# Kernel tuning notes

Hardware: AMD Instinct MI355X
Metric: run time of the kernel (lower is better)

The kernel has to match this reference:

```python
import jax, jax.numpy as jnp
import numpy as np
from jax import lax

N_CLASS = 32000
N_HIDDEN = 512
S_ENC = 1024
S_DEC = 256


def setup_inputs() -> dict:
    key = jax.random.key(0)
    ks = jax.random.split(key, 16)
    C, H = N_CLASS, N_HIDDEN
    sC = np.float32(1.0 / np.sqrt(C))
    sH = np.float32(1.0 / np.sqrt(H))
    f32 = jnp.float32
    return {
        "encoder_inputs": jax.random.normal(ks[0], (1, S_ENC, C), f32),
        "hidden_0": jnp.zeros((1, 1, H), f32),
        "decoder_inputs": jax.random.normal(ks[1], (1, S_DEC, C), f32),
        # encoder RNN params (torch nn.RNN layout: W_ih [H,C], W_hh [H,H])
        "enc_Wih": jax.random.normal(ks[2], (H, C), f32) * sC,
        "enc_Whh": jax.random.normal(ks[3], (H, H), f32) * sH,
        "enc_bih": jax.random.normal(ks[4], (H,), f32) * sH,
        "enc_bhh": jax.random.normal(ks[5], (H,), f32) * sH,
        # decoder RNN params
        "dec_Wih": jax.random.normal(ks[6], (H, C), f32) * sC,
        "dec_Whh": jax.random.normal(ks[7], (H, H), f32) * sH,
        "dec_bih": jax.random.normal(ks[8], (H,), f32) * sH,
        "dec_bhh": jax.random.normal(ks[9], (H,), f32) * sH,
        # attention Linear [H,H]
        "attn_W": jax.random.normal(ks[10], (H, H), f32) * sH,
        "attn_b": jax.random.normal(ks[11], (H,), f32) * sH,
        # output Linear [C, 2H]
        "out_W": jax.random.normal(ks[12], (C, 2 * H), f32) * sH,
        "out_b": jax.random.normal(ks[13], (C,), f32) * sH,
    }


def _rnn_scan(x, h0, Wih, Whh, bih, bhh):
    # x: [S, C], h0: [H] -> hs: [S, H], hT: [H]  (tanh vanilla RNN)
    def step(h, xt):
        h = jnp.tanh(xt @ Wih.T + bih + h @ Whh.T + bhh)
        return h, h
    hT, hs = lax.scan(step, h0, x)
    return hs, hT


def reference(encoder_inputs, hidden_0, decoder_inputs,
              enc_Wih, enc_Whh, enc_bih, enc_bhh,
              dec_Wih, dec_Whh, dec_bih, dec_bhh,
              attn_W, attn_b, out_W, out_b):
    enc_x = encoder_inputs[0]   # [S_enc, C] (batch=1)
    dec_x = decoder_inputs[0]   # [S_dec, C]
    h0 = hidden_0[0, 0]         # [H]

    enc_hs, enc_hT = _rnn_scan(enc_x, h0, enc_Wih, enc_Whh, enc_bih, enc_bhh)

    # score_i = dot(dec_h, attn(enc_h_i)); precompute attn over all encoder states
    attn_enc = enc_hs @ attn_W.T + attn_b   # [S_enc, H]

    def dec_step(h, xt):
        h = jnp.tanh(xt @ dec_Wih.T + dec_bih + h @ dec_Whh.T + dec_bhh)  # [H]
        w = jax.nn.softmax(attn_enc @ h)      # [S_enc]
        context = w @ enc_hs                  # [H]
        out = jnp.concatenate([h, context]) @ out_W.T + out_b  # [C]
        return h, (out, w)

    _, (outputs, attn) = lax.scan(dec_step, enc_hT, dec_x)
    # outputs: [S_dec, n_class], attn: [S_dec, S_enc]
    return outputs, attn
```

## Files before the change

kernel.cpp:

```cpp
#include <hip/hip_runtime.h>

typedef _Float16 f16;
typedef _Float16 f16x2 __attribute__((ext_vector_type(2)));
typedef _Float16 f16x8 __attribute__((ext_vector_type(8)));
typedef float f32x4 __attribute__((ext_vector_type(4)));

#define NCLS 32000
#define NH   512
#define SE   1024
#define SD   256

static __device__ __forceinline__ f16x2 h2bc(unsigned int x) {
  return __builtin_bit_cast(f16x2, x);
}

static __device__ __forceinline__ float fdot2f(f16x2 a, f16x2 b, float c) {
#if __has_builtin(__builtin_amdgcn_fdot2)
  return __builtin_amdgcn_fdot2(a, b, c, false);
#else
  return c + (float)a[0]*(float)b[0] + (float)a[1]*(float)b[1];
#endif
}

static __device__ __forceinline__ uint4 gload16(const void* p) {
  uint4 r;
  asm volatile("global_load_dwordx4 %0, %1, off" : "=v"(r) : "v"(p));
  return r;
}
static __device__ __forceinline__ void waitvm0() {
  asm volatile("s_waitcnt vmcnt(0)" ::: "memory");
  __builtin_amdgcn_sched_barrier(0);
}

__global__ void k_cvt2(const float* __restrict__ s0, f16* __restrict__ d0,
                       const float* __restrict__ s1, f16* __restrict__ d1, int n) {
  int i = blockIdx.x*blockDim.x + threadIdx.x;
  int st = gridDim.x*blockDim.x;
  for (; i < 2*n; i += st) {
    if (i < n) d0[i] = (f16)s0[i];
    else       d1[i-n] = (f16)s1[i-n];
  }
}

template<int AF32, int BF32>
__global__ __launch_bounds__(1024, 4) void k_gemm6(
    const void* __restrict__ A0v, const void* __restrict__ B0v,
    f16* __restrict__ P0, float* __restrict__ C0, int M0, int gy0, int ldc0, int nb0,
    const void* __restrict__ A1v, const void* __restrict__ B1v,
    f16* __restrict__ P1, float* __restrict__ C1, int M1, int gy1, int ldc1,
    int gx, int lda, int ldb, const float* __restrict__ bias, int kLen)
{
  __shared__ f16 S[2][2][256][40];
  int tid = threadIdx.x;
  int lane = tid & 63;
  int wid = tid >> 6;
  int wr = wid >> 2, wc = wid & 3;

  int nwg = gridDim.x;
  int d = blockIdx.x;
  int q = nwg >> 3, rm = nwg & 7, xcd = d & 7, lin = d >> 3;
  int L = (xcd < rm ? xcd*(q+1) : rm*(q+1) + (xcd-rm)*q) + lin;

  const void* Av; const void* Bv; f16* P16; float* C32; int M, gy, ldc; int lid;
  if (L < nb0) { Av=A0v; Bv=B0v; P16=P0; C32=C0; M=M0; gy=gy0; ldc=ldc0; lid=L; }
  else { Av=A1v; Bv=B1v; P16=P1; C32=C1; M=M1; gy=gy1; ldc=ldc1; lid=L-nb0; }
  int gxy = gx*gy;
  int bz = lid / gxy; int rr2 = lid % gxy;
  int by = rr2 / gx, bx = rr2 % gx;

  long row0 = (long)by*256, col0 = (long)bx*256;
  long k0 = (long)bz*kLen;

  bool isA = tid < 512;
  int t2 = isA ? tid : tid - 512;
  int r = t2 >> 1, koff = (t2 & 1) * 16;

  const float* pf = nullptr; const f16* ph = nullptr;
  if (isA) {
    if constexpr (AF32) pf = (const float*)Av + (row0 + r)*(long)lda + k0 + koff;
    else                ph = (const f16*)Av  + (row0 + r)*(long)lda + k0 + koff;
  } else {
    if constexpr (BF32) pf = (const float*)Bv + (col0 + r)*(long)ldb + k0 + koff;
    else                ph = (const f16*)Bv  + (col0 + r)*(long)ldb + k0 + koff;
  }
  bool srcF = isA ? (AF32 != 0) : (BF32 != 0);

  f32x4 fa[4];
  uint4 ha[2];
  int nst = kLen >> 5;

#define G_LOAD(T) do { long gk = (long)(T)*32;                                  \
    if (srcF) { const f32x4* p = (const f32x4*)(pf + gk);                       \
      fa[0]=p[0]; fa[1]=p[1]; fa[2]=p[2]; fa[3]=p[3]; }                         \
    else { const uint4* p = (const uint4*)(ph + gk); ha[0]=p[0]; ha[1]=p[1]; }  \
  } while(0)

#define G_STORE(B) do {                                                         \
    f16* dst = &S[B][isA?0:1][r][koff];                                         \
    if (srcF) { f16x8 h0, h1;                                                   \
      _Pragma("unroll") for (int qq=0;qq<4;qq++){                               \
        h0[qq]=(f16)fa[0][qq]; h0[4+qq]=(f16)fa[1][qq];                         \
        h1[qq]=(f16)fa[2][qq]; h1[4+qq]=(f16)fa[3][qq]; }                       \
      *(f16x8*)dst = h0; *(f16x8*)(dst+8) = h1; }                               \
    else { *(uint4*)dst = ha[0]; *(uint4*)(dst+8) = ha[1]; }                    \
  } while(0)

  f32x4 acc[4][4];
  #pragma unroll
  for (int i=0;i<4;i++)
    #pragma unroll
    for (int j=0;j<4;j++)
      acc[i][j] = (f32x4){0.f,0.f,0.f,0.f};

  G_LOAD(0);
  G_STORE(0);
  __syncthreads();

  int cur = 0;
  for (int t = 0; t < nst; ++t) {
    if (t+1 < nst) G_LOAD(t+1);

    f16x8 a[4], b[4];
    #pragma unroll
    for (int i=0;i<4;i++)
      a[i] = *(const f16x8*)&S[cur][0][wr*64 + i*16 + (lane&15)][(lane>>4)*8];
    #pragma unroll
    for (int j=0;j<4;j++)
      b[j] = *(const f16x8*)&S[cur][1][wc*64 + j*16 + (lane&15)][(lane>>4)*8];
    #pragma unroll
    for (int i=0;i<4;i++)
      #pragma unroll
      for (int j=0;j<4;j++)
        acc[i][j] = __builtin_amdgcn_mfma_f32_16x16x32_f16(a[i], b[j], acc[i][j], 0,0,0);

    if (t+1 < nst) G_STORE(cur^1);
    __syncthreads();
    cur ^= 1;
  }

  if (P16) {
    long base = (long)bz * M;
    #pragma unroll
    for (int i=0;i<4;i++)
      #pragma unroll
      for (int j=0;j<4;j++)
        #pragma unroll
        for (int v=0;v<4;v++) {
          long row = row0 + wr*64 + i*16 + ((lane>>4)*4) + v;
          long col = col0 + wc*64 + j*16 + (lane&15);
          P16[(base + row)*(long)ldc + col] = (f16)acc[i][j][v];
        }
  } else {
    #pragma unroll
    for (int i=0;i<4;i++)
      #pragma unroll
      for (int j=0;j<4;j++)
        #pragma unroll
        for (int v=0;v<4;v++) {
          long row = row0 + wr*64 + i*16 + ((lane>>4)*4) + v;
          long col = col0 + wc*64 + j*16 + (lane&15);
          float val = acc[i][j][v];
          if (bias) val += bias[col];
          C32[row*(long)ldc + col] = val;
        }
  }
#undef G_LOAD
#undef G_STORE
}

__global__ __launch_bounds__(512, 4) void k_gemm7(
    const f16* __restrict__ A16, int lda, const float* __restrict__ B32, int ldb,
    float* __restrict__ C32, int ldc, const float* __restrict__ bias, int kLen)
{
  __shared__ f16 SA[2][256][40];
  __shared__ f16 SB[2][64][40];
  int tid = threadIdx.x;
  int lane = tid & 63;
  int wid = tid >> 6;
  int wr = wid >> 1, wc = wid & 1;

  int nwg = gridDim.x, d = blockIdx.x;
  int q = nwg >> 3, rm = nwg & 7, xcd = d & 7, lin = d >> 3;
  int L = (xcd < rm ? xcd*(q+1) : rm*(q+1) + (xcd-rm)*q) + lin;
  long col0 = (long)L * 64;

  int ra0 = tid >> 2,        ka0 = (tid & 3) * 8;
  int ra1 = (tid+512) >> 2,  ka1 = ((tid+512) & 3) * 8;
  int rb  = tid >> 3,        kb  = (tid & 7) * 4;

  const f16*   pA0 = A16 + (long)ra0*lda + ka0;
  const f16*   pA1 = A16 + (long)ra1*lda + ka1;
  const float* pB  = B32 + (col0 + rb)*(long)ldb + kb;

  uint4 ha0, ha1; f32x4 fb;
  int nst = kLen >> 5;

#define G_LOAD(T) do { long gk = (long)(T)*32;                                  \
    ha0 = *(const uint4*)(pA0 + gk);                                            \
    ha1 = *(const uint4*)(pA1 + gk);                                            \
    fb  = *(const f32x4*)(pB + gk);                                             \
  } while(0)

#define G_STORE(Bf) do {                                                        \
    *(uint4*)&SA[Bf][ra0][ka0] = ha0;                                           \
    *(uint4*)&SA[Bf][ra1][ka1] = ha1;                                           \
    f16x2 h0; h0[0]=(f16)fb[0]; h0[1]=(f16)fb[1];                               \
    f16x2 h1; h1[0]=(f16)fb[2]; h1[1]=(f16)fb[3];                               \
    *(f16x2*)&SB[Bf][rb][kb] = h0;                                              \
    *(f16x2*)&SB[Bf][rb][kb+2] = h1;                                            \
  } while(0)

  f32x4 acc[4][2];
  #pragma unroll
  for (int i=0;i<4;i++)
    #pragma unroll
    for (int j=0;j<2;j++)
      acc[i][j] = (f32x4){0.f,0.f,0.f,0.f};

  G_LOAD(0);
  G_STORE(0);
  __syncthreads();

  int cur = 0;
  for (int t = 0; t < nst; ++t) {
    if (t+1 < nst) G_LOAD(t+1);

    f16x8 a[4], b[2];
    #pragma unroll
    for (int i=0;i<4;i++)
      a[i] = *(const f16x8*)&SA[cur][wr*64 + i*16 + (lane&15)][(lane>>4)*8];
    #pragma unroll
    for (int j=0;j<2;j++)
      b[j] = *(const f16x8*)&SB[cur][wc*32 + j*16 + (lane&15)][(lane>>4)*8];
    #pragma unroll
    for (int i=0;i<4;i++)
      #pragma unroll
      for (int j=0;j<2;j++)
        acc[i][j] = __builtin_amdgcn_mfma_f32_16x16x32_f16(a[i], b[j], acc[i][j], 0,0,0);

    if (t+1 < nst) G_STORE(cur^1);
    __syncthreads();
    cur ^= 1;
  }

  #pragma unroll
  for (int i=0;i<4;i++)
    #pragma unroll
    for (int j=0;j<2;j++)
      #pragma unroll
      for (int v=0;v<4;v++) {
        long row = wr*64 + i*16 + ((lane>>4)*4) + v;
        long col = col0 + wc*32 + j*16 + (lane&15);
        C32[row*(long)ldc + col] = acc[i][j][v] + bias[col];
      }
#undef G_LOAD
#undef G_STORE
}

template<int AF32, int BF32>
__global__ __launch_bounds__(256, 4) void k_gemm3(
    const void* __restrict__ Av, int lda, const void* __restrict__ Bv, int ldb,
    float* __restrict__ C32, f16* __restrict__ C16, int ldc,
    const float* __restrict__ bias, int M, int kLen)
{
  __shared__ f16 At[2][64][72];
  __shared__ f16 Bt[2][64][72];
  int tid = threadIdx.x;
  int lane = tid & 63;
  int wid = tid >> 6;
  int wr = wid >> 1, wc = wid & 1;

  int gx = gridDim.x, gy = gridDim.y;
  int d = blockIdx.x + gx*(blockIdx.y + gy*blockIdx.z);
  int nwg = gx*gy*gridDim.z;
  int q = nwg >> 3, rm = nwg & 7, xcd = d & 7, lin = d >> 3;
  int L = (xcd < rm ? xcd*(q+1) : rm*(q+1) + (xcd-rm)*q) + lin;
  int bx = L % gx; int rem = L / gx;
  int by = rem % gy; int bz = rem / gy;

  long row0 = (long)by*64, col0 = (long)bx*64;
  long k0 = (long)bz*kLen;

  const float* A32 = (const float*)Av; const f16* A16 = (const f16*)Av;
  const float* B32 = (const float*)Bv; const f16* B16 = (const f16*)Bv;

  int r = tid >> 2, koff = (tid & 3) * 16;

  const float* pAf = A32 + (row0 + r)*(long)lda + k0 + koff;
  const float* pBf = B32 + (col0 + r)*(long)ldb + k0 + koff;
  const f16*   pAh = A16 + (row0 + r)*(long)lda + k0 + koff;
  const f16*   pBh = B16 + (col0 + r)*(long)ldb + k0 + koff;

  f32x4 fa[4], fb[4];
  uint4 ha[2], hb[2];

  int nst = kLen >> 6;

#define G_LOAD(T) do { long gk = (long)(T)*64;                                  \
    if constexpr (AF32) { const f32x4* p = (const f32x4*)(pAf + gk);            \
      fa[0]=p[0]; fa[1]=p[1]; fa[2]=p[2]; fa[3]=p[3]; }                         \
    else { const uint4* p = (const uint4*)(pAh + gk); ha[0]=p[0]; ha[1]=p[1]; } \
    if constexpr (BF32) { const f32x4* p = (const f32x4*)(pBf + gk);            \
      fb[0]=p[0]; fb[1]=p[1]; fb[2]=p[2]; fb[3]=p[3]; }                         \
    else { const uint4* p = (const uint4*)(pBh + gk); hb[0]=p[0]; hb[1]=p[1]; } \
  } while(0)

#define G_STORE(B) do {                                                         \
    if constexpr (AF32) { f16x8 h0, h1;                                         \
      _Pragma("unroll") for (int qq=0;qq<4;qq++){                               \
        h0[qq]=(f16)fa[0][qq]; h0[4+qq]=(f16)fa[1][qq];                         \
        h1[qq]=(f16)fa[2][qq]; h1[4+qq]=(f16)fa[3][qq]; }                       \
      *(f16x8*)&At[B][r][koff] = h0; *(f16x8*)&At[B][r][koff+8] = h1; }         \
    else { *(uint4*)&At[B][r][koff] = ha[0]; *(uint4*)&At[B][r][koff+8] = ha[1]; } \
    if constexpr (BF32) { f16x8 h2, h3;                                         \
      _Pragma("unroll") for (int qq=0;qq<4;qq++){                               \
        h2[qq]=(f16)fb[0][qq]; h2[4+qq]=(f16)fb[1][qq];                         \
        h3[qq]=(f16)fb[2][qq]; h3[4+qq]=(f16)fb[3][qq]; }                       \
      *(f16x8*)&Bt[B][r][koff] = h2; *(f16x8*)&Bt[B][r][koff+8] = h3; }         \
    else { *(uint4*)&Bt[B][r][koff] = hb[0]; *(uint4*)&Bt[B][r][koff+8] = hb[1]; } \
  } while(0)

  f32x4 acc[2][2];
  #pragma unroll
  for (int i=0;i<2;i++)
    #pragma unroll
    for (int j=0;j<2;j++)
      acc[i][j] = (f32x4){0.f,0.f,0.f,0.f};

  G_LOAD(0);
  G_STORE(0);
  __syncthreads();

  int cur = 0;
  for (int t = 0; t < nst; ++t) {
    if (t+1 < nst) G_LOAD(t+1);

    f16x8 a[2][2], b[2][2];
    #pragma unroll
    for (int kk=0;kk<2;kk++) {
      #pragma unroll
      for (int i=0;i<2;i++)
        a[kk][i] = *(const f16x8*)&At[cur][wr*32 + i*16 + (lane&15)][kk*32 + (lane>>4)*8];
      #pragma unroll
      for (int j=0;j<2;j++)
        b[kk][j] = *(const f16x8*)&Bt[cur][wc*32 + j*16 + (lane&15)][kk*32 + (lane>>4)*8];
    }
    #pragma unroll
    for (int kk=0;kk<2;kk++)
      #pragma unroll
      for (int i=0;i<2;i++)
        #pragma unroll
        for (int j=0;j<2;j++)
          acc[i][j] = __builtin_amdgcn_mfma_f32_16x16x32_f16(a[kk][i], b[kk][j], acc[i][j], 0,0,0);

    if (t+1 < nst) G_STORE(cur^1);
    __syncthreads();
    cur ^= 1;
  }

  long zofs = (long)bz * (long)M * (long)ldc;
  #pragma unroll
  for (int i=0;i<2;i++)
    #pragma unroll
    for (int j=0;j<2;j++)
      #pragma unroll
      for (int v=0;v<4;v++) {
        long row = row0 + wr*32 + i*16 + ((lane>>4)*4) + v;
        long col = col0 + wc*32 + j*16 + (lane&15);
        float val = acc[i][j][v];
        if (bias) val += bias[col];
        if (C32) C32[zofs + row*(long)ldc + col] = val;
        else     C16[row*(long)ldc + col] = (f16)val;
      }
#undef G_LOAD
#undef G_STORE
}

__global__ void k_reduceh2(
    const f16* __restrict__ pE, float* __restrict__ oE,
    const float* __restrict__ be1, const float* __restrict__ be2, int MNe,
    const f16* __restrict__ pD, float* __restrict__ oD,
    const float* __restrict__ bd1, const float* __restrict__ bd2, int MNd,
    int S, int nbE)
{
  const f16* part; float* out; const float* b1; const float* b2; int MN, i;
  if ((int)blockIdx.x < nbE) {
    part = pE; out = oE; b1 = be1; b2 = be2; MN = MNe;
    i = (blockIdx.x*256 + threadIdx.x)*4;
  } else {
    part = pD; out = oD; b1 = bd1; b2 = bd2; MN = MNd;
    i = ((blockIdx.x-nbE)*256 + threadIdx.x)*4;
  }
  if (i >= MN) return;
  float s0=0.f, s1=0.f, s2=0.f, s3=0.f;
  for (int z = 0; z < S; ++z) {
    uint2 v = *(const uint2*)(part + (long)z*MN + i);
    f16x2 lo = h2bc(v.x), hi = h2bc(v.y);
    s0 += (float)lo[0]; s1 += (float)lo[1];
    s2 += (float)hi[0]; s3 += (float)hi[1];
  }
  out[i+0] = s0 + b1[(i+0)&511] + b2[(i+0)&511];
  out[i+1] = s1 + b1[(i+1)&511] + b2[(i+1)&511];
  out[i+2] = s2 + b1[(i+2)&511] + b2[(i+2)&511];
  out[i+3] = s3 + b1[(i+3)&511] + b2[(i+3)&511];
}

__global__ void k_reduce16(const float* __restrict__ part, f16* __restrict__ out,
                           int ld, int S, int MN, int N) {
  int i = blockIdx.x*256 + threadIdx.x;
  if (i >= MN) return;
  float s = 0.f;
  for (int z = 0; z < S; ++z) s += part[(long)z*MN + i];
  out[(long)(i / N)*ld + (i % N)] = (f16)s;
}

__global__ __launch_bounds__(256) void k_gemm_f32(
    const float* __restrict__ A, int lda,
    const float* __restrict__ B, const float* __restrict__ B2,
    const float* __restrict__ bk, int ldb,
    float* __restrict__ C, int ldc, int kLen, int M)
{
  __shared__ float As[64][33], Bs[64][33];
  int tid = threadIdx.x;
  int r0 = blockIdx.x*64, c0 = blockIdx.y*64;
  long zk = (long)blockIdx.z * kLen;
  int ty = tid >> 4, tx = tid & 15;
  float acc[4][4];
  #pragma unroll
  for (int i=0;i<4;i++)
    #pragma unroll
    for (int j=0;j<4;j++) acc[i][j] = 0.f;
  int sr = tid >> 2, skq = (tid & 3) * 8;
  for (int k0 = 0; k0 < kLen; k0 += 32) {
    __syncthreads();
    long ao = (long)(r0+sr)*lda + zk + k0 + skq;
    long bo = (long)(c0+sr)*ldb + zk + k0 + skq;
    float4 a0 = *(const float4*)&A[ao];
    float4 a1 = *(const float4*)&A[ao + 4];
    float4 b0 = *(const float4*)&B[bo];
    float4 b1 = *(const float4*)&B[bo + 4];
    if (B2) {
      float4 c0v = *(const float4*)&B2[bo];
      float4 c1v = *(const float4*)&B2[bo + 4];
      float4 k0v = *(const float4*)&bk[zk + k0 + skq];
      float4 k1v = *(const float4*)&bk[zk + k0 + skq + 4];
      b0.x += c0v.x + k0v.x; b0.y += c0v.y + k0v.y;
      b0.z += c0v.z + k0v.z; b0.w += c0v.w + k0v.w;
      b1.x += c1v.x + k1v.x; b1.y += c1v.y + k1v.y;
      b1.z += c1v.z + k1v.z; b1.w += c1v.w + k1v.w;
    }
    As[sr][skq+0]=a0.x; As[sr][skq+1]=a0.y; As[sr][skq+2]=a0.z; As[sr][skq+3]=a0.w;
    As[sr][skq+4]=a1.x; As[sr][skq+5]=a1.y; As[sr][skq+6]=a1.z; As[sr][skq+7]=a1.w;
    Bs[sr][skq+0]=b0.x; Bs[sr][skq+1]=b0.y; Bs[sr][skq+2]=b0.z; Bs[sr][skq+3]=b0.w;
    Bs[sr][skq+4]=b1.x; Bs[sr][skq+5]=b1.y; Bs[sr][skq+6]=b1.z; Bs[sr][skq+7]=b1.w;
    __syncthreads();
    #pragma unroll
    for (int k=0;k<32;k++) {
      float av[4], bv[4];
      #pragma unroll
      for (int i=0;i<4;i++) av[i] = As[ty*4+i][k];
      #pragma unroll
      for (int j=0;j<4;j++) bv[j] = Bs[tx*4+j][k];
      #pragma unroll
      for (int i=0;i<4;i++)
        #pragma unroll
        for (int j=0;j<4;j++) acc[i][j] += av[i]*bv[j];
    }
  }
  long zofs = (long)blockIdx.z * (long)M * (long)ldc;
  #pragma unroll
  for (int i=0;i<4;i++)
    #pragma unroll
    for (int j=0;j<4;j++) {
      int row = r0 + ty*4 + i, col = c0 + tx*4 + j;
      C[zofs + (long)row*ldc + col] = acc[i][j];
    }
}

__global__ __launch_bounds__(512)
__attribute__((amdgpu_waves_per_eu(1))) void k_scan3(
    const float* __restrict__ encpre,
    const float* __restrict__ decpre,
    const f16* __restrict__ WE, const f16* __restrict__ WD,
    const float* __restrict__ seed,
    float* __restrict__ ehs32, f16* __restrict__ ehsT, int ldT,
    float* __restrict__ dhs32, f16* __restrict__ dA, int ldA,
    int GE, int CH, int WARM)
{
  __shared__ uint4 wl[2][8][512];
  __shared__ f16 hbuf[2][512];
  int tid = threadIdx.x;
  int rj = tid & 7, ri = tid >> 3;

  uint4 wv[6][8];

#define LOADW(Wp) do { const f16* _wb = (Wp);                                   \
    _Pragma("unroll") for (int rr=0; rr<6; ++rr)                                \
      _Pragma("unroll") for (int jb=0; jb<8; ++jb)                              \
        wv[rr][jb] = gload16(_wb + ((ri*8+rr)*512 + rj*64 + jb*8));             \
    _Pragma("unroll") for (int rr=0; rr<2; ++rr)                                \
      _Pragma("unroll") for (int jb=0; jb<8; ++jb)                              \
        wl[rr][jb][tid] =                                                       \
            *(const uint4*)(_wb + ((ri*8+6+rr)*512 + rj*64 + jb*8));            \
  } while(0)

  int g = blockIdx.x;
  long uout = (g < GE) ? (long)g*CH : 1024 + (long)(g-GE)*CH;
  long uend = uout + CH;
  long u0 = uout - WARM; if (u0 < 0) u0 = 0;

  LOADW(u0 < 1024 ? WE : WD);

  {
    float h0v = seed[tid];
    int b = tid >> 3, w = tid & 7;
    int pb = ((b&7)<<3) | (b>>3);
    hbuf[0][pb*8 + w] = (f16)h0v;
  }
  waitvm0();
  __syncthreads();

  int cur = 0;

  auto step = [&](const float* __restrict__ prerow, int isenc, long u) {
    float pv = prerow[tid];
    const f16* hb = hbuf[cur];
    float acc[8] = {0.f,0.f,0.f,0.f,0.f,0.f,0.f,0.f};
    #pragma unroll
    for (int jb=0; jb<8; ++jb) {
      uint4 hv = *(const uint4*)(hb + (((jb<<3)|rj)<<3));
      f16x2 hp0 = h2bc(hv.x), hp1 = h2bc(hv.y), hp2 = h2bc(hv.z), hp3 = h2bc(hv.w);
      #pragma unroll
      for (int rr=0; rr<6; ++rr) {
        uint4 wp = wv[rr][jb];
        acc[rr] = fdot2f(h2bc(wp.x), hp0, acc[rr]);
        acc[rr] = fdot2f(h2bc(wp.y), hp1, acc[rr]);
        acc[rr] = fdot2f(h2bc(wp.z), hp2, acc[rr]);
        acc[rr] = fdot2f(h2bc(wp.w), hp3, acc[rr]);
      }
      uint4 w6 = wl[0][jb][tid];
      acc[6] = fdot2f(h2bc(w6.x), hp0, acc[6]);
      acc[6] = fdot2f(h2bc(w6.y), hp1, acc[6]);
      acc[6] = fdot2f(h2bc(w6.z), hp2, acc[6]);
      acc[6] = fdot2f(h2bc(w6.w), hp3, acc[6]);
      uint4 w7 = wl[1][jb][tid];
      acc[7] = fdot2f(h2bc(w7.x), hp0, acc[7]);
      acc[7] = fdot2f(h2bc(w7.y), hp1, acc[7]);
      acc[7] = fdot2f(h2bc(w7.z), hp2, acc[7]);
      acc[7] = fdot2f(h2bc(w7.w), hp3, acc[7]);
    }
    int b2 = rj & 4, b1 = rj & 2, b0 = rj & 1;
    float t4[4];
    #pragma unroll
    for (int k=0;k<4;k++) {
      float keep = b2 ? acc[4+k] : acc[k];
      float send = b2 ? acc[k]   : acc[4+k];
      t4[k] = keep + __shfl_xor(send, 4);
    }
    float t2[2];
    #pragma unroll
    for (int k=0;k<2;k++) {
      float keep = b1 ? t4[2+k] : t4[k];
      float send = b1 ? t4[k]   : t4[2+k];
      t2[k] = keep + __shfl_xor(send, 2);
    }
    float keep = b0 ? t2[1] : t2[0];
    float send = b0 ? t2[0] : t2[1];
    float tot = keep + __shfl_xor(send, 1);

    float s = tot + pv;
    float ex = __expf(2.f*s);
    float h = 1.f - 2.f/(ex + 1.f);

    {
      int b = tid >> 3, w = tid & 7;
      int pb = ((b&7)<<3) | (b>>3);
      hbuf[cur^1][pb*8 + w] = (f16)h;
    }
    if (u >= uout) {
      if (isenc) {
        ehs32[u*512 + tid] = h;
        ehsT[(long)tid*ldT + u] = (f16)h;
      } else {
        long td = u - 1024;
        dhs32[td*512 + tid] = h;
        dA[td*(long)ldA + tid] = (f16)h;
      }
    }
    cur ^= 1;
    __syncthreads();
  };

  long u = u0;
  long e1 = uend < 1024 ? uend : 1024;
  for (; u < e1; ++u) step(encpre + u*512, 1, u);
  if (u < uend && u0 < 1024) {
    LOADW(WD);
    waitvm0();
    __syncthreads();
  }
  for (; u < uend; ++u) step(decpre + (u-1024)*512, 0, u);
#undef LOADW
}

__global__ __launch_bounds__(256) void k_softmax(const float* __restrict__ SP,
    float* __restrict__ outw, f16* __restrict__ probs, int S)
{
  int row = blockIdx.x, tid = threadIdx.x;
  int lane = tid & 63, wid = tid >> 6;
  __shared__ float red[4];
  float v[4];
  #pragma unroll
  for (int k=0;k<4;k++) {
    long o = (long)row*1024 + tid + k*256;
    float s = 0.f;
    for (int z = 0; z < S; ++z) s += SP[(long)z*256*1024 + o];
    v[k] = s;
  }
  float m = fmaxf(fmaxf(v[0],v[1]), fmaxf(v[2],v[3]));
  #pragma unroll
  for (int d=32; d; d>>=1) m = fmaxf(m, __shfl_xor(m, d));
  if (lane==0) red[wid] = m;
  __syncthreads();
  m = fmaxf(fmaxf(red[0],red[1]), fmaxf(red[2],red[3]));
  float e[4], s = 0.f;
  #pragma unroll
  for (int k=0;k<4;k++) { e[k] = __expf(v[k]-m); s += e[k]; }
  #pragma unroll
  for (int d=32; d; d>>=1) s += __shfl_xor(s, d);
  __syncthreads();
  if (lane==0) red[wid] = s;
  __syncthreads();
  s = red[0]+red[1]+red[2]+red[3];
  float inv = 1.f/s;
  #pragma unroll
  for (int k=0;k<4;k++) {
    int c = tid + k*256;
    float w = e[k]*inv;
    outw[(long)row*1024 + c] = w;
    probs[(long)row*1024 + c] = (f16)w;
  }
}

extern "C" void kernel_launch(void* const* d_in, const int* in_sizes, int n_in,
                              void* d_out, int out_size, void* d_ws, size_t ws_size,
                              hipStream_t stream) {
  const float* enc_x = (const float*)d_in[0];
  const float* h0    = (const float*)d_in[1];
  const float* dec_x = (const float*)d_in[2];
  const float* eWih  = (const float*)d_in[3];
  const float* eWhh  = (const float*)d_in[4];
  const float* ebih  = (const float*)d_in[5];
  const float* ebhh  = (const float*)d_in[6];
  const float* dWih  = (const float*)d_in[7];
  const float* dWhh  = (const float*)d_in[8];
  const float* dbih  = (const float*)d_in[9];
  const float* dbhh  = (const float*)d_in[10];
  const float* aW    = (const float*)d_in[11];
  const float* ab    = (const float*)d_in[12];
  const float* oW    = (const float*)d_in[13];
  const float* ob    = (const float*)d_in[14];

  float* out0 = (float*)d_out;
  float* out1 = out0 + (size_t)SD*NCLS;

  f16* o_partE = (f16*)out0;
  f16* o_partD = (f16*)((char*)d_out + 26214400);

  char* ws = (char*)d_ws;
  f16*   o_concatA16 = (f16*)  (ws + 0);
  char*  A           = ws + 524288;
  float* o_encpre    = (float*)(A + 0);
  float* o_decpre    = (float*)(A + 2097152);
  f16*   o_WhhE      = (f16*)  (A + 2621440);
  f16*   o_WhhD      = (f16*)  (A + 3145728);
  float* o_enchs32   = (float*)(A + 3670016);
  f16*   o_enchsT16  = (f16*)  (A + 5767168);
  float* o_dechs32   = (float*)(A + 8912896);
  f16*   o_probs16   = (f16*)  (A + 10485760);
  float* o_ctxpart   = (float*)(A + 11010048);
  float* o_aepart    = (float*)(A + 13107200);
  float* o_scpart    = (float*)(A + 17301504);

  k_cvt2<<<1024,256,0,stream>>>(eWhh, o_WhhE, dWhh, o_WhhD, 512*512);

  k_gemm6<1,1><<<250,1024,0,stream>>>(
      enc_x, eWih, o_partE, nullptr, 1024, 4, 512, 200,
      dec_x, dWih, o_partD, nullptr, 256, 1, 512,
      2, NCLS, NCLS, nullptr, 1280);
  k_reduceh2<<<640,256,0,stream>>>(
      o_partE, o_encpre, ebih, ebhh, 1024*512,
      o_partD, o_decpre, dbih, dbhh, 256*512, 25, 512);

  k_scan3<<<160,512,0,stream>>>(o_encpre, o_decpre, o_WhhE, o_WhhD, h0,
      o_enchs32, o_enchsT16, 1024,
      o_dechs32, o_concatA16, 1024,
      128, 8, 24);

  k_gemm_f32<<<dim3(16,8,2),256,0,stream>>>(o_enchs32, 512,
      aW, nullptr, nullptr, 512, o_aepart, 512, 256, 1024);

  k_gemm_f32<<<dim3(4,16,4),256,0,stream>>>(o_dechs32, 512,
      o_aepart, o_aepart + (size_t)1024*512, ab, 512, o_scpart, 1024, 128, 256);

  k_softmax<<<256,256,0,stream>>>(o_scpart, out1, o_probs16, 4);

  k_gemm3<0,0><<<dim3(8,4,4),256,0,stream>>>(o_probs16, 1024, o_enchsT16, 1024,
      o_ctxpart, nullptr, 512, nullptr, 256, 256);
  k_reduce16<<<512,256,0,stream>>>(o_ctxpart, o_concatA16 + 512, 1024, 4, 256*512, 512);

  k_gemm7<<<500,512,0,stream>>>(o_concatA16, 1024, oW, 1024,
      out0, NCLS, ob, 1024);
}
```

Before: 301.7 us.

## Reassociate attention scores via transposed attn weight and run them as f16 GEMMs

Scores are now computed as (dec_h · W_attn) · enc_hs^T rather than dec_h · (enc_hs · W_attn^T + b)^T. The attention bias term is dropped, which is valid because it adds the same constant to every score in a row and cancels in the softmax. The weight is transposed and cast to f16 in the prep kernel, and both products now use the existing f16 gemm3 kernel instead of the scalar fp32 GEMM. The scan writes only f16 hidden states, so the fp32 copies and the split-K partial reduction are removed. The trade-off is lower score precision with f16 inputs on small kernels within a long pipeline.

```diff
diff --git a/kernel.cpp b/kernel.cpp
--- a/kernel.cpp
+++ b/kernel.cpp
@@ -32,13 +32,20 @@
   __builtin_amdgcn_sched_barrier(0);
 }
 
-__global__ void k_cvt2(const float* __restrict__ s0, f16* __restrict__ d0,
-                       const float* __restrict__ s1, f16* __restrict__ d1, int n) {
+__global__ void k_prep(const float* __restrict__ eW, f16* __restrict__ dE,
+                       const float* __restrict__ dW, f16* __restrict__ dD,
+                       const float* __restrict__ aW, f16* __restrict__ Wt,
+                       int n) {
   int i = blockIdx.x*blockDim.x + threadIdx.x;
   int st = gridDim.x*blockDim.x;
-  for (; i < 2*n; i += st) {
-    if (i < n) d0[i] = (f16)s0[i];
-    else       d1[i-n] = (f16)s1[i-n];
+  for (; i < 3*n; i += st) {
+    if (i < n)        dE[i] = (f16)eW[i];
+    else if (i < 2*n) dD[i-n] = (f16)dW[i-n];
+    else {
+      int j = i - 2*n;
+      int m = j >> 9, k = j & 511;
+      Wt[j] = (f16)aW[(k << 9) | m];
+    }
   }
 }
 
@@ -414,77 +421,15 @@
   out[(long)(i / N)*ld + (i % N)] = (f16)s;
 }
 
-__global__ __launch_bounds__(256) void k_gemm_f32(
-    const float* __restrict__ A, int lda,
-    const float* __restrict__ B, const float* __restrict__ B2,
-    const float* __restrict__ bk, int ldb,
-    float* __restrict__ C, int ldc, int kLen, int M)
-{
-  __shared__ float As[64][33], Bs[64][33];
-  int tid = threadIdx.x;
-  int r0 = blockIdx.x*64, c0 = blockIdx.y*64;
-  long zk = (long)blockIdx.z * kLen;
-  int ty = tid >> 4, tx = tid & 15;
-  float acc[4][4];
-  #pragma unroll
-  for (int i=0;i<4;i++)
-    #pragma unroll
-    for (int j=0;j<4;j++) acc[i][j] = 0.f;
-  int sr = tid >> 2, skq = (tid & 3) * 8;
-  for (int k0 = 0; k0 < kLen; k0 += 32) {
-    __syncthreads();
-    long ao = (long)(r0+sr)*lda + zk + k0 + skq;
-    long bo = (long)(c0+sr)*ldb + zk + k0 + skq;
-    float4 a0 = *(const float4*)&A[ao];
-    float4 a1 = *(const float4*)&A[ao + 4];
-    float4 b0 = *(const float4*)&B[bo];
-    float4 b1 = *(const float4*)&B[bo + 4];
-    if (B2) {
-      float4 c0v = *(const float4*)&B2[bo];
-      float4 c1v = *(const float4*)&B2[bo + 4];
-      float4 k0v = *(const float4*)&bk[zk + k0 + skq];
-      float4 k1v = *(const float4*)&bk[zk + k0 + skq + 4];
-      b0.x += c0v.x + k0v.x; b0.y += c0v.y + k0v.y;
-      b0.z += c0v.z + k0v.z; b0.w += c0v.w + k0v.w;
-      b1.x += c1v.x + k1v.x; b1.y += c1v.y + k1v.y;
-      b1.z += c1v.z + k1v.z; b1.w += c1v.w + k1v.w;
-    }
-    As[sr][skq+0]=a0.x; As[sr][skq+1]=a0.y; As[sr][skq+2]=a0.z; As[sr][skq+3]=a0.w;
-    As[sr][skq+4]=a1.x; As[sr][skq+5]=a1.y; As[sr][skq+6]=a1.z; As[sr][skq+7]=a1.w;
-    Bs[sr][skq+0]=b0.x; Bs[sr][skq+1]=b0.y; Bs[sr][skq+2]=b0.z; Bs[sr][skq+3]=b0.w;
-    Bs[sr][skq+4]=b1.x; Bs[sr][skq+5]=b1.y; Bs[sr][skq+6]=b1.z; Bs[sr][skq+7]=b1.w;
-    __syncthreads();
-    #pragma unroll
-    for (int k=0;k<32;k++) {
-      float av[4], bv[4];
-      #pragma unroll
-      for (int i=0;i<4;i++) av[i] = As[ty*4+i][k];
-      #pragma unroll
-      for (int j=0;j<4;j++) bv[j] = Bs[tx*4+j][k];
-      #pragma unroll
-      for (int i=0;i<4;i++)
-        #pragma unroll
-        for (int j=0;j<4;j++) acc[i][j] += av[i]*bv[j];
-    }
-  }
-  long zofs = (long)blockIdx.z * (long)M * (long)ldc;
-  #pragma unroll
-  for (int i=0;i<4;i++)
-    #pragma unroll
-    for (int j=0;j<4;j++) {
-      int row = r0 + ty*4 + i, col = c0 + tx*4 + j;
-      C[zofs + (long)row*ldc + col] = acc[i][j];
-    }
-}
-
 __global__ __launch_bounds__(512)
 __attribute__((amdgpu_waves_per_eu(1))) void k_scan3(
     const float* __restrict__ encpre,
     const float* __restrict__ decpre,
     const f16* __restrict__ WE, const f16* __restrict__ WD,
     const float* __restrict__ seed,
-    float* __restrict__ ehs32, f16* __restrict__ ehsT, int ldT,
-    float* __restrict__ dhs32, f16* __restrict__ dA, int ldA,
+    f16* __restrict__ ehs16,
+    f16* __restrict__ ehsT, int ldT,
+    f16* __restrict__ dA, int ldA,
     int GE, int CH, int WARM)
 {
   __shared__ uint4 wl[2][8][512];
@@ -571,20 +516,20 @@
     float s = tot + pv;
     float ex = __expf(2.f*s);
     float h = 1.f - 2.f/(ex + 1.f);
+    f16 h16 = (f16)h;
 
     {
       int b = tid >> 3, w = tid & 7;
       int pb = ((b&7)<<3) | (b>>3);
-      hbuf[cur^1][pb*8 + w] = (f16)h;
+      hbuf[cur^1][pb*8 + w] = h16;
     }
     if (u >= uout) {
       if (isenc) {
-        ehs32[u*512 + tid] = h;
-        ehsT[(long)tid*ldT + u] = (f16)h;
+        ehs16[u*512 + tid] = h16;
+        ehsT[(long)tid*ldT + u] = h16;
       } else {
         long td = u - 1024;
-        dhs32[td*512 + tid] = h;
-        dA[td*(long)ldA + tid] = (f16)h;
+        dA[td*(long)ldA + tid] = h16;
       }
     }
     cur ^= 1;
@@ -603,20 +548,15 @@
 #undef LOADW
 }
 
-__global__ __launch_bounds__(256) void k_softmax(const float* __restrict__ SP,
-    float* __restrict__ outw, f16* __restrict__ probs, int S)
+__global__ __launch_bounds__(256) void k_softmax(const float* __restrict__ S,
+    float* __restrict__ outw, f16* __restrict__ probs)
 {
   int row = blockIdx.x, tid = threadIdx.x;
   int lane = tid & 63, wid = tid >> 6;
   __shared__ float red[4];
   float v[4];
   #pragma unroll
-  for (int k=0;k<4;k++) {
-    long o = (long)row*1024 + tid + k*256;
-    float s = 0.f;
-    for (int z = 0; z < S; ++z) s += SP[(long)z*256*1024 + o];
-    v[k] = s;
-  }
+  for (int k=0;k<4;k++) v[k] = S[(long)row*1024 + tid + k*256];
   float m = fmaxf(fmaxf(v[0],v[1]), fmaxf(v[2],v[3]));
   #pragma unroll
   for (int d=32; d; d>>=1) m = fmaxf(m, __shfl_xor(m, d));
@@ -657,7 +597,6 @@
   const float* dbih  = (const float*)d_in[9];
   const float* dbhh  = (const float*)d_in[10];
   const float* aW    = (const float*)d_in[11];
-  const float* ab    = (const float*)d_in[12];
   const float* oW    = (const float*)d_in[13];
   const float* ob    = (const float*)d_in[14];
 
@@ -669,20 +608,20 @@
 
   char* ws = (char*)d_ws;
   f16*   o_concatA16 = (f16*)  (ws + 0);
-  char*  A           = ws + 524288;
-  float* o_encpre    = (float*)(A + 0);
-  float* o_decpre    = (float*)(A + 2097152);
-  f16*   o_WhhE      = (f16*)  (A + 2621440);
-  f16*   o_WhhD      = (f16*)  (A + 3145728);
-  float* o_enchs32   = (float*)(A + 3670016);
-  f16*   o_enchsT16  = (f16*)  (A + 5767168);
-  float* o_dechs32   = (float*)(A + 8912896);
-  f16*   o_probs16   = (f16*)  (A + 10485760);
-  float* o_ctxpart   = (float*)(A + 11010048);
-  float* o_aepart    = (float*)(A + 13107200);
-  float* o_scpart    = (float*)(A + 17301504);
-
-  k_cvt2<<<1024,256,0,stream>>>(eWhh, o_WhhE, dWhh, o_WhhD, 512*512);
+  f16*   o_WhhE      = (f16*)  (ws + 524288);
+  f16*   o_WhhD      = (f16*)  (ws + 1048576);
+  f16*   o_WtT16     = (f16*)  (ws + 1572864);
+  char*  B           = ws + 2097152;
+  float* o_encpre    = (float*)(B + 0);
+  float* o_decpre    = (float*)(B + 2097152);
+  f16*   o_ehs16     = (f16*)  (B + 2621440);
+  f16*   o_enchsT16  = (f16*)  (B + 3670016);
+  f16*   o_v16       = (f16*)  (B + 4718592);
+  f16*   o_probs16   = (f16*)  (B + 4980736);
+  float* o_scores    = (float*)(B + 5505024);
+  float* o_ctxpart   = (float*)(B + 6553600);
+
+  k_prep<<<1024,256,0,stream>>>(eWhh, o_WhhE, dWhh, o_WhhD, aW, o_WtT16, 512*512);
 
   k_gemm6<1,1><<<250,1024,0,stream>>>(
       enc_x, eWih, o_partE, nullptr, 1024, 4, 512, 200,
@@ -693,17 +632,17 @@
       o_partD, o_decpre, dbih, dbhh, 256*512, 25, 512);
 
   k_scan3<<<160,512,0,stream>>>(o_encpre, o_decpre, o_WhhE, o_WhhD, h0,
-      o_enchs32, o_enchsT16, 1024,
-      o_dechs32, o_concatA16, 1024,
+      o_ehs16, o_enchsT16, 1024,
+      o_concatA16, 1024,
       128, 8, 24);
 
-  k_gemm_f32<<<dim3(16,8,2),256,0,stream>>>(o_enchs32, 512,
-      aW, nullptr, nullptr, 512, o_aepart, 512, 256, 1024);
-
-  k_gemm_f32<<<dim3(4,16,4),256,0,stream>>>(o_dechs32, 512,
-      o_aepart, o_aepart + (size_t)1024*512, ab, 512, o_scpart, 1024, 128, 256);
-
-  k_softmax<<<256,256,0,stream>>>(o_scpart, out1, o_probs16, 4);
+  k_gemm3<0,0><<<dim3(8,4,1),256,0,stream>>>(o_concatA16, 1024, o_WtT16, 512,
+      nullptr, o_v16, 512, nullptr, 256, 512);
+
+  k_gemm3<0,0><<<dim3(16,4,1),256,0,stream>>>(o_v16, 512, o_ehs16, 512,
+      o_scores, nullptr, 1024, nullptr, 256, 512);
+
+  k_softmax<<<256,256,0,stream>>>(o_scores, out1, o_probs16);
 
   k_gemm3<0,0><<<dim3(8,4,4),256,0,stream>>>(o_probs16, 1024, o_enchsT16, 1024,
       o_ctxpart, nullptr, 512, nullptr, 256, 256);
```

Measured after the change: 293.3 us (median of 2 runs). -2.8%, faster.
